# Kernel optimization log

Measured on AMD Instinct MI355X. Metric: run time of the kernel, lower is better.

The kernel has to match this reference:

```python
import jax, jax.numpy as jnp
import numpy as np

B, L, D, H, NS = 8, 1024, 64, 16, 3
DH = D // H          # head dim = 4 (scale = sqrt(4) = 2, matching K_.size(-1)**0.5)
DFF = 4 * D          # 256
EPS = 1e-5


def _bn(x_bld, gamma, beta):
    # BatchNorm1d in training mode on (B, C, L): normalize per-channel over (B, L)
    mean = jnp.mean(x_bld, axis=(0, 1))          # [D]
    var = jnp.mean((x_bld - mean) ** 2, axis=(0, 1))  # biased variance, as torch uses
    return gamma * (x_bld - mean) / jnp.sqrt(var + EPS) + beta


def setup_inputs() -> dict:
    key = jax.random.key(0)
    ks = jax.random.split(key, 12)
    s = 0.05
    inp = {
        "x": jax.random.normal(ks[0], (B, L, D), dtype=jnp.float32),
        # W_embed: Conv1d(64,64,k=1) == linear over channels
        "W_embed": jax.random.normal(ks[1], (D, D), dtype=jnp.float32) * s,
        "b_embed": jnp.zeros((D,), dtype=jnp.float32),
        "g0": jnp.ones((D,), dtype=jnp.float32),
        "be0": jnp.zeros((D,), dtype=jnp.float32),
        # shared attention weights (reused every stack)
        "Wq": jax.random.normal(ks[2], (D, D), dtype=jnp.float32) * s,
        "bq": jnp.zeros((D,), dtype=jnp.float32),
        "Wk": jax.random.normal(ks[3], (D, D), dtype=jnp.float32) * s,
        "bk": jnp.zeros((D,), dtype=jnp.float32),
        "Wv": jax.random.normal(ks[4], (D, D), dtype=jnp.float32) * s,
        "bv": jnp.zeros((D,), dtype=jnp.float32),
        "g_attn": jnp.ones((D,), dtype=jnp.float32),
        "be_attn": jnp.zeros((D,), dtype=jnp.float32),
        # shared feedforward (1x1 convs == channel linears)
        "W1": jax.random.normal(ks[5], (DFF, D), dtype=jnp.float32) * s,
        "b1": jnp.zeros((DFF,), dtype=jnp.float32),
        "W2": jax.random.normal(ks[6], (D, DFF), dtype=jnp.float32) * s,
        "b2": jnp.zeros((D,), dtype=jnp.float32),
        "g_ff": jnp.ones((D,), dtype=jnp.float32),
        "be_ff": jnp.zeros((D,), dtype=jnp.float32),
    }
    return inp


def reference(x, W_embed, b_embed, g0, be0, Wq, bq, Wk, bk, Wv, bv,
              g_attn, be_attn, W1, b1, W2, b2, g_ff, be_ff):
    # input embedding (1x1 conv) + batchnorm
    enc = x @ W_embed.T + b_embed              # [B, L, D]
    enc = _bn(enc, g0, be0)

    for _ in range(NS):  # num_stacks, SAME weights each stack (as in source)
        # --- multi-head attention (ReLU-activated QKV projections) ---
        Q = jax.nn.relu(enc @ Wq.T + bq)        # [B, L, D]
        K = jax.nn.relu(enc @ Wk.T + bk)
        V = jax.nn.relu(enc @ Wv.T + bv)
        q = Q.reshape(B, L, H, DH)
        k = K.reshape(B, L, H, DH)
        v = V.reshape(B, L, H, DH)
        scores = jnp.einsum('blhd,bmhd->bhlm', q, k) / jnp.sqrt(jnp.float32(DH))
        A = jax.nn.softmax(scores, axis=-1)     # [B, H, L, L]
        o = jnp.einsum('bhlm,bmhd->blhd', A, v).reshape(B, L, D)
        o = o + enc                             # residual
        enc = _bn(o, g_attn, be_attn)

        # --- feedforward: conv1d(k=1) -> ReLU -> conv1d(k=1) -> ReLU, residual, BN ---
        h = jax.nn.relu(enc @ W1.T + b1)        # [B, L, 4D]
        h = jax.nn.relu(h @ W2.T + b2)          # [B, L, D]
        h = h + enc                             # residual
        enc = _bn(h, g_ff, be_ff)
    return enc
```

## Files before the change

### kernel.cpp

```cpp
#include <hip/hip_runtime.h>
#include <math.h>

static constexpr int B_ = 8, L_ = 1024, D_ = 64, H_ = 16, DH_ = 4, DFF_ = 256;
static constexpr int M_ = B_ * L_;
static constexpr float EPS_ = 1e-5f;
static constexpr float INV_N_ = 1.0f / (float)M_;
static constexpr int PSTR_ = 128;

typedef _Float16 half4_ __attribute__((ext_vector_type(4)));
typedef __fp16   fp16x2 __attribute__((ext_vector_type(2)));
typedef float    f32x4  __attribute__((ext_vector_type(4)));

__global__ __launch_bounds__(256) void prep_kernel(
    const float* __restrict__ we, const float* __restrict__ wq,
    const float* __restrict__ wk, const float* __restrict__ wv,
    const float* __restrict__ w1, const float* __restrict__ w2,
    _Float16* __restrict__ dst)
{
    int e = blockIdx.x * 256 + threadIdx.x;
    float v;
    if      (e <  4096) v = we[e];
    else if (e <  8192) v = wq[e - 4096];
    else if (e < 12288) v = wk[e - 8192];
    else if (e < 16384) v = wv[e - 12288];
    else if (e < 32768) v = w1[e - 16384];
    else                v = w2[e - 32768];
    dst[e] = (_Float16)v;
}

template<int KT, int AF16, int BN_A, int RELU, int RESID_BN, int STATS, int OUTF16>
__device__ __forceinline__ void linear_mfma(
    const float* __restrict__ Af, const _Float16* __restrict__ Ah,
    const _Float16* __restrict__ Wh,
    const float* __restrict__ bias, const float* __restrict__ resid,
    float* __restrict__ Cf, _Float16* __restrict__ Ch, float outScale,
    int N, int m0, int n0,
    const float* __restrict__ partsIn, int npb,
    const float* __restrict__ gg, const float* __restrict__ bb,
    float* __restrict__ outParts, int blkIdx)
{
    constexpr int CPR = KT / 4;
    __shared__ half4_ Alds[64][CPR + 1];
    __shared__ half4_ Wlds[64][CPR + 1];
    __shared__ float  raw[128];
    __shared__ float  bnsc[64], bnsh[64];
    __shared__ float  wstats[4][128];
    const int t = threadIdx.x;

    if (BN_A || RESID_BN) {
        if (t < 128) {
            const float* pr = partsIn + (size_t)t * PSTR_;
            float a = 0.f;
            for (int j = 0; j < npb; j += 4) {
                float4 v4 = *(const float4*)&pr[j];
                a += v4.x + v4.y + v4.z + v4.w;
            }
            raw[t] = a;
        }
        __syncthreads();
        if (t < 64) {
            float mean = raw[t] * INV_N_;
            float ex2  = raw[64 + t] * INV_N_;
            float rs   = rsqrtf(ex2 - mean * mean + EPS_);
            float s2   = gg[t] * rs;
            bnsc[t] = s2;
            bnsh[t] = bb[t] - mean * s2;
        }
        __syncthreads();
    }

    {
        constexpr int ITERS = (64 * CPR) / 256;
        #pragma unroll
        for (int i = 0; i < ITERS; ++i) {
            int l = i * 256 + t;
            int row = l / CPR, c4 = l % CPR;
            half4_ hv;
            if (AF16) {
                hv = *(const half4_*)&Ah[(size_t)(m0 + row) * KT + c4 * 4];
            } else {
                float4 av = *(const float4*)&Af[(size_t)(m0 + row) * KT + c4 * 4];
                if (BN_A) {
                    int c = c4 * 4;
                    av.x = fmaf(av.x, bnsc[c + 0], bnsh[c + 0]);
                    av.y = fmaf(av.y, bnsc[c + 1], bnsh[c + 1]);
                    av.z = fmaf(av.z, bnsc[c + 2], bnsh[c + 2]);
                    av.w = fmaf(av.w, bnsc[c + 3], bnsh[c + 3]);
                }
                hv = half4_{(_Float16)av.x, (_Float16)av.y,
                            (_Float16)av.z, (_Float16)av.w};
            }
            Alds[row][c4] = hv;
            Wlds[row][c4] = *(const half4_*)&Wh[(size_t)(n0 + row) * KT + c4 * 4];
        }
    }
    __syncthreads();

    const int lane = t & 63, w = t >> 6, g = lane >> 4, ml = lane & 15;

    f32x4 acc[4] = {};
    #pragma unroll
    for (int kci = 0; kci < KT / 16; ++kci) {
        half4_ af = Alds[w * 16 + ml][kci * 4 + g];
        #pragma unroll
        for (int nt = 0; nt < 4; ++nt) {
            half4_ wf = Wlds[nt * 16 + ml][kci * 4 + g];
            acc[nt] = __builtin_amdgcn_mfma_f32_16x16x16f16(wf, af, acc[nt], 0, 0, 0);
        }
    }

    const int m = m0 + w * 16 + ml;
    float sv[4][4], qv[4][4];
    #pragma unroll
    for (int nt = 0; nt < 4; ++nt) {
        const int cb = nt * 16 + 4 * g;
        const int nc = n0 + cb;
        float4 bv4 = *(const float4*)&bias[nc];
        float r0 = acc[nt][0] + bv4.x, r1 = acc[nt][1] + bv4.y;
        float r2 = acc[nt][2] + bv4.z, r3 = acc[nt][3] + bv4.w;
        if (RELU) {
            r0 = fmaxf(r0, 0.f); r1 = fmaxf(r1, 0.f);
            r2 = fmaxf(r2, 0.f); r3 = fmaxf(r3, 0.f);
        }
        if (RESID_BN) {
            float4 rv = *(const float4*)&resid[(size_t)m * N + nc];
            r0 += fmaf(rv.x, bnsc[cb + 0], bnsh[cb + 0]);
            r1 += fmaf(rv.y, bnsc[cb + 1], bnsh[cb + 1]);
            r2 += fmaf(rv.z, bnsc[cb + 2], bnsh[cb + 2]);
            r3 += fmaf(rv.w, bnsc[cb + 3], bnsh[cb + 3]);
        }
        if (OUTF16) {
            half4_ hs = { (_Float16)(r0 * outScale), (_Float16)(r1 * outScale),
                          (_Float16)(r2 * outScale), (_Float16)(r3 * outScale) };
            *(half4_*)&Ch[(size_t)m * N + nc] = hs;
        } else {
            float4 o4 = { r0, r1, r2, r3 };
            *(float4*)&Cf[(size_t)m * N + nc] = o4;
        }
        if (STATS) {
            sv[nt][0] = r0; sv[nt][1] = r1; sv[nt][2] = r2; sv[nt][3] = r3;
            qv[nt][0] = r0 * r0; qv[nt][1] = r1 * r1;
            qv[nt][2] = r2 * r2; qv[nt][3] = r3 * r3;
        }
    }

    if (STATS) {
        #pragma unroll
        for (int d = 1; d <= 8; d <<= 1)
            #pragma unroll
            for (int nt = 0; nt < 4; ++nt)
                #pragma unroll
                for (int r = 0; r < 4; ++r) {
                    sv[nt][r] += __shfl_xor(sv[nt][r], d);
                    qv[nt][r] += __shfl_xor(qv[nt][r], d);
                }
        if (ml == 0) {
            #pragma unroll
            for (int nt = 0; nt < 4; ++nt)
                #pragma unroll
                for (int r = 0; r < 4; ++r) {
                    int ch = nt * 16 + 4 * g + r;
                    wstats[w][ch]      = sv[nt][r];
                    wstats[w][64 + ch] = qv[nt][r];
                }
        }
        __syncthreads();
        if (t < 128) {
            float a = wstats[0][t] + wstats[1][t] + wstats[2][t] + wstats[3][t];
            outParts[(size_t)t * PSTR_ + blkIdx] = a;
        }
    }
}

__global__ __launch_bounds__(256) void embed_kernel(
    const float* __restrict__ x, const _Float16* __restrict__ wemh,
    const float* __restrict__ bias, float* __restrict__ C,
    float* __restrict__ outParts)
{
    linear_mfma<64, 0, 0, 0, 0, 1, 0>(x, nullptr, wemh, bias, nullptr,
                                      C, nullptr, 1.f, 64, blockIdx.x * 64, 0,
                                      nullptr, 0, nullptr, nullptr,
                                      outParts, blockIdx.x);
}

__global__ __launch_bounds__(256) void qkv_kernel(
    const float* __restrict__ tmpA,
    const _Float16* __restrict__ wqh, const float* __restrict__ bq,
    const _Float16* __restrict__ wkh, const float* __restrict__ bk,
    const _Float16* __restrict__ wvh, const float* __restrict__ bv,
    _Float16* __restrict__ qh, _Float16* __restrict__ kh, _Float16* __restrict__ vh,
    const float* __restrict__ partsIn,
    const float* __restrict__ g, const float* __restrict__ be)
{
    const _Float16* W; const float* bias; _Float16* C; float sc2;
    if (blockIdx.y == 0)      { W = wqh; bias = bq; C = qh; sc2 = 0.5f; }
    else if (blockIdx.y == 1) { W = wkh; bias = bk; C = kh; sc2 = 1.f; }
    else                      { W = wvh; bias = bv; C = vh; sc2 = 1.f; }
    linear_mfma<64, 0, 1, 1, 0, 0, 1>(tmpA, nullptr, W, bias, nullptr,
                                      nullptr, C, sc2, 64, blockIdx.x * 64, 0,
                                      partsIn, 128, g, be, nullptr, 0);
}

__global__ __launch_bounds__(256) void ff1_kernel(
    const float* __restrict__ tmpB, const _Float16* __restrict__ w1h,
    const float* __restrict__ b1, _Float16* __restrict__ h1,
    const float* __restrict__ partsB,
    const float* __restrict__ g, const float* __restrict__ be)
{
    linear_mfma<64, 0, 1, 1, 0, 0, 1>(tmpB, nullptr, w1h, b1, nullptr,
                                      nullptr, h1, 1.f, 256,
                                      blockIdx.x * 64, blockIdx.y * 64,
                                      partsB, 64, g, be, nullptr, 0);
}

__global__ __launch_bounds__(256) void ff2_kernel(
    const _Float16* __restrict__ h1, const _Float16* __restrict__ w2h,
    const float* __restrict__ b2, const float* __restrict__ tmpB,
    float* __restrict__ tmpA, const float* __restrict__ partsB,
    const float* __restrict__ g, const float* __restrict__ be,
    float* __restrict__ partsOut)
{
    linear_mfma<256, 1, 0, 1, 1, 1, 0>(nullptr, h1, w2h, b2, tmpB,
                                       tmpA, nullptr, 1.f, 64, blockIdx.x * 64, 0,
                                       partsB, 64, g, be, partsOut, blockIdx.x);
}

__global__ __launch_bounds__(256) void attn_kernel(
    const _Float16* __restrict__ q, const _Float16* __restrict__ k,
    const _Float16* __restrict__ v, const float* __restrict__ encRaw,
    float* __restrict__ out, const float* __restrict__ partsIn,
    const float* __restrict__ gPrev, const float* __restrict__ bPrev,
    float* __restrict__ partsOut)
{
    __shared__ half4_   klds[1024];
    __shared__ _Float16 vstage[4][1040];
    __shared__ half4_   vlds[1024];
    __shared__ float    raw8[8], rsc[4], rsh[4];
    __shared__ float    wred[4][8];

    const int bid = blockIdx.x;
    const int qc  = bid & 7;
    const int h   = (bid >> 3) & 15;
    const int b   = bid >> 7;
    const int t   = threadIdx.x;

    if (t < 8) {
        const int row = (t >> 2) * 64 + 4 * h + (t & 3);
        const float* pr = partsIn + (size_t)row * PSTR_;
        float a = 0.f;
        for (int j = 0; j < 128; j += 4) {
            float4 v4 = *(const float4*)&pr[j];
            a += v4.x + v4.y + v4.z + v4.w;
        }
        raw8[t] = a;
    }

    const size_t baseh = (size_t)b * (L_ * D_) + h * DH_;

    #pragma unroll
    for (int i = 0; i < 4; ++i) {
        int key = i * 256 + t;
        klds[key] = *(const half4_*)&k[baseh + (size_t)key * D_];
        half4_ vv = *(const half4_*)&v[baseh + (size_t)key * D_];
        vstage[0][key] = vv[0]; vstage[1][key] = vv[1];
        vstage[2][key] = vv[2]; vstage[3][key] = vv[3];
    }
    __syncthreads();

    if (t < 4) {
        float mean = raw8[t] * INV_N_;
        float ex2  = raw8[4 + t] * INV_N_;
        float rs   = rsqrtf(ex2 - mean * mean + EPS_);
        float s2   = gPrev[4 * h + t] * rs;
        rsc[t] = s2;
        rsh[t] = bPrev[4 * h + t] - mean * s2;
    }

    #pragma unroll
    for (int i = 0; i < 4; ++i) {
        int e = i * 256 + t;
        int d = e & 3, g2 = (e >> 2) & 3, c = e >> 4;
        int k0 = c * 16 + g2 * 4;
        half4_ hv = { vstage[d][k0 + 0], vstage[d][k0 + 1],
                      vstage[d][k0 + 2], vstage[d][k0 + 3] };
        vlds[e] = hv;
    }
    __syncthreads();

    const int lane = t & 63;
    const int wv2  = t >> 6;
    const int ln16 = lane & 15;
    const int g16  = lane >> 4;
    const int q0   = qc * 128 + wv2 * 32;

    half4_ qf0 = { 0, 0, 0, 0 }, qf1 = { 0, 0, 0, 0 };
    if (lane < 16) {
        qf0 = *(const half4_*)&q[(size_t)(b * L_ + q0 + ln16) * D_ + h * DH_];
        qf1 = *(const half4_*)&q[(size_t)(b * L_ + q0 + 16 + ln16) * D_ + h * DH_];
    }

    const half4_ ones = { (_Float16)1.f, (_Float16)1.f, (_Float16)1.f, (_Float16)1.f };
    const f32x4  fz   = { 0.f, 0.f, 0.f, 0.f };
    f32x4 o0 = fz, o1 = fz;

    #pragma unroll 2
    for (int c = 0; c < 64; ++c) {
        half4_ ka = klds[c * 16 + ln16];
        half4_ va = vlds[c * 16 + g16 * 4 + (ln16 & 3)];
        if (ln16 == 4) va = ones;

        f32x4 s0 = __builtin_amdgcn_mfma_f32_16x16x16f16(ka, qf0, fz, 0, 0, 0);
        f32x4 s1 = __builtin_amdgcn_mfma_f32_16x16x16f16(ka, qf1, fz, 0, 0, 0);

        float e00 = __expf(s0[0]), e01 = __expf(s0[1]);
        float e02 = __expf(s0[2]), e03 = __expf(s0[3]);
        float e10 = __expf(s1[0]), e11 = __expf(s1[1]);
        float e12 = __expf(s1[2]), e13 = __expf(s1[3]);

        fp16x2 a0 = __builtin_amdgcn_cvt_pkrtz(e00, e01);
        fp16x2 b0 = __builtin_amdgcn_cvt_pkrtz(e02, e03);
        fp16x2 a1 = __builtin_amdgcn_cvt_pkrtz(e10, e11);
        fp16x2 b1 = __builtin_amdgcn_cvt_pkrtz(e12, e13);
        half4_ p0 = __builtin_bit_cast(half4_, __builtin_shufflevector(a0, b0, 0, 1, 2, 3));
        half4_ p1 = __builtin_bit_cast(half4_, __builtin_shufflevector(a1, b1, 0, 1, 2, 3));

        o0 = __builtin_amdgcn_mfma_f32_16x16x16f16(va, p0, o0, 0, 0, 0);
        o1 = __builtin_amdgcn_mfma_f32_16x16x16f16(va, p1, o1, 0, 0, 0);
    }

    float ls0 = __shfl(o0[0], 16 + ln16);
    float ls1 = __shfl(o1[0], 16 + ln16);

    float4 r0v = { 0.f, 0.f, 0.f, 0.f }, r1v = r0v;
    if (lane < 16) {
        {
            const size_t gi = (size_t)(b * L_ + q0 + ln16) * D_ + h * DH_;
            const float inv = 1.0f / ls0;
            const float4 e4 = *(const float4*)&encRaw[gi];
            r0v.x = fmaf(o0[0], inv, fmaf(e4.x, rsc[0], rsh[0]));
            r0v.y = fmaf(o0[1], inv, fmaf(e4.y, rsc[1], rsh[1]));
            r0v.z = fmaf(o0[2], inv, fmaf(e4.z, rsc[2], rsh[2]));
            r0v.w = fmaf(o0[3], inv, fmaf(e4.w, rsc[3], rsh[3]));
            *(float4*)&out[gi] = r0v;
        }
        {
            const size_t gi = (size_t)(b * L_ + q0 + 16 + ln16) * D_ + h * DH_;
            const float inv = 1.0f / ls1;
            const float4 e4 = *(const float4*)&encRaw[gi];
            r1v.x = fmaf(o1[0], inv, fmaf(e4.x, rsc[0], rsh[0]));
            r1v.y = fmaf(o1[1], inv, fmaf(e4.y, rsc[1], rsh[1]));
            r1v.z = fmaf(o1[2], inv, fmaf(e4.z, rsc[2], rsh[2]));
            r1v.w = fmaf(o1[3], inv, fmaf(e4.w, rsc[3], rsh[3]));
            *(float4*)&out[gi] = r1v;
        }
    }

    float s4[4] = { r0v.x + r1v.x, r0v.y + r1v.y, r0v.z + r1v.z, r0v.w + r1v.w };
    float q4[4] = { r0v.x*r0v.x + r1v.x*r1v.x, r0v.y*r0v.y + r1v.y*r1v.y,
                    r0v.z*r0v.z + r1v.z*r1v.z, r0v.w*r0v.w + r1v.w*r1v.w };
    #pragma unroll
    for (int d2 = 1; d2 <= 8; d2 <<= 1) {
        #pragma unroll
        for (int j = 0; j < 4; ++j) {
            s4[j] += __shfl_xor(s4[j], d2);
            q4[j] += __shfl_xor(q4[j], d2);
        }
    }
    if (lane == 0) {
        #pragma unroll
        for (int j = 0; j < 4; ++j) { wred[wv2][j] = s4[j]; wred[wv2][4 + j] = q4[j]; }
    }
    __syncthreads();
    if (t < 8) {
        float a = wred[0][t] + wred[1][t] + wred[2][t] + wred[3][t];
        const int row = (t >> 2) * 64 + 4 * h + (t & 3);
        partsOut[(size_t)row * PSTR_ + (b * 8 + qc)] = a;
    }
}

__global__ __launch_bounds__(256) void bn_apply_kernel(
    const float* __restrict__ x, const float* __restrict__ parts,
    const float* __restrict__ gamma, const float* __restrict__ beta,
    float* __restrict__ y)
{
    __shared__ float fstats[128];
    const int t = threadIdx.x;
    if (t < 128) {
        const float* pr = parts + (size_t)t * PSTR_;
        float a = 0.f;
        for (int j = 0; j < 128; j += 4) {
            float4 v4 = *(const float4*)&pr[j];
            a += v4.x + v4.y + v4.z + v4.w;
        }
        fstats[t] = a;
    }
    __syncthreads();

    const int idx = blockIdx.x * 256 + t;
    const int c = (idx & 15) << 2;
    float4 xv = ((const float4*)x)[idx];
    float4 sm = *(const float4*)&fstats[c];
    float4 sq = *(const float4*)&fstats[64 + c];
    float4 g  = *(const float4*)&gamma[c];
    float4 be = *(const float4*)&beta[c];

    float mean[4] = {sm.x * INV_N_, sm.y * INV_N_, sm.z * INV_N_, sm.w * INV_N_};
    float ex2[4]  = {sq.x * INV_N_, sq.y * INV_N_, sq.z * INV_N_, sq.w * INV_N_};
    float xa[4] = {xv.x, xv.y, xv.z, xv.w};
    float ga[4] = {g.x, g.y, g.z, g.w};
    float ba[4] = {be.x, be.y, be.z, be.w};
    float ya[4];
    #pragma unroll
    for (int i = 0; i < 4; ++i) {
        float var = ex2[i] - mean[i] * mean[i];
        float rs = rsqrtf(var + EPS_);
        ya[i] = ga[i] * (xa[i] - mean[i]) * rs + ba[i];
    }
    float4 r = {ya[0], ya[1], ya[2], ya[3]};
    ((float4*)y)[idx] = r;
}

extern "C" void kernel_launch(void* const* d_in, const int* in_sizes, int n_in,
                              void* d_out, int out_size, void* d_ws, size_t ws_size,
                              hipStream_t stream)
{
    const float* x       = (const float*)d_in[0];
    const float* W_embed = (const float*)d_in[1];
    const float* b_embed = (const float*)d_in[2];
    const float* g0      = (const float*)d_in[3];
    const float* be0     = (const float*)d_in[4];
    const float* Wq      = (const float*)d_in[5];
    const float* bq      = (const float*)d_in[6];
    const float* Wk      = (const float*)d_in[7];
    const float* bk      = (const float*)d_in[8];
    const float* Wv      = (const float*)d_in[9];
    const float* bv      = (const float*)d_in[10];
    const float* g_attn  = (const float*)d_in[11];
    const float* be_attn = (const float*)d_in[12];
    const float* W1      = (const float*)d_in[13];
    const float* b1      = (const float*)d_in[14];
    const float* W2      = (const float*)d_in[15];
    const float* b2      = (const float*)d_in[16];
    const float* g_ff    = (const float*)d_in[17];
    const float* be_ff   = (const float*)d_in[18];

    float* ws     = (float*)d_ws;
    float* tmpA   = ws;
    float* tmpB   = ws + 524288;
    float* partsA = ws + 1048576;
    float* partsB = ws + 1064960;
    _Float16* hb  = (_Float16*)(ws + 1081344);
    _Float16* qh  = hb;
    _Float16* kh  = hb + 524288;
    _Float16* vh  = hb + 1048576;
    _Float16* h1  = hb + 1572864;
    _Float16* wemh = hb + 3670016;
    _Float16* wqh  = wemh + 4096;
    _Float16* wkh  = wqh + 4096;
    _Float16* wvh  = wkh + 4096;
    _Float16* w1h  = wvh + 4096;
    _Float16* w2h  = w1h + 16384;
    float* out = (float*)d_out;

    const dim3 blk(256);

    prep_kernel<<<192, blk, 0, stream>>>(W_embed, Wq, Wk, Wv, W1, W2, wemh);
    embed_kernel<<<128, blk, 0, stream>>>(x, wemh, b_embed, tmpA, partsA);

    for (int s = 0; s < 3; ++s) {
        const float* gP  = (s == 0) ? g0  : g_ff;
        const float* beP = (s == 0) ? be0 : be_ff;
        qkv_kernel<<<dim3(128, 3), blk, 0, stream>>>(
            tmpA, wqh, bq, wkh, bk, wvh, bv, qh, kh, vh, partsA, gP, beP);
        attn_kernel<<<1024, blk, 0, stream>>>(
            qh, kh, vh, tmpA, tmpB, partsA, gP, beP, partsB);
        ff1_kernel<<<dim3(128, 4), blk, 0, stream>>>(
            tmpB, w1h, b1, h1, partsB, g_attn, be_attn);
        ff2_kernel<<<128, blk, 0, stream>>>(
            h1, w2h, b2, tmpB, tmpA, partsB, g_attn, be_attn, partsA);
    }
    bn_apply_kernel<<<512, blk, 0, stream>>>(tmpA, partsA, g_ff, be_ff, out);
}
```

Measured before the change: 189.0 us.

## Fuse feedforward linears into one kernel keeping hidden activations in registers

Merges the two feedforward 1x1-conv kernels into a single kernel. The first MFMA output is bias+ReLU'd and packed directly as the A operand of the second MFMA. This removes the global round trip of the 4D-wide hidden tensor and one launch per stack. Weights are read from global/cache rather than staged in LDS. The residual is taken from the fp16 normalized tile in LDS, trading some precision, and only 128 blocks are launched.

```diff
diff --git a/kernel.cpp b/kernel.cpp
--- a/kernel.cpp
+++ b/kernel.cpp
@@ -28,11 +28,10 @@
     dst[e] = (_Float16)v;
 }
 
-template<int KT, int AF16, int BN_A, int RELU, int RESID_BN, int STATS, int OUTF16>
+template<int KT, int BN_A, int RELU, int STATS, int OUTF16>
 __device__ __forceinline__ void linear_mfma(
-    const float* __restrict__ Af, const _Float16* __restrict__ Ah,
-    const _Float16* __restrict__ Wh,
-    const float* __restrict__ bias, const float* __restrict__ resid,
+    const float* __restrict__ Af, const _Float16* __restrict__ Wh,
+    const float* __restrict__ bias,
     float* __restrict__ Cf, _Float16* __restrict__ Ch, float outScale,
     int N, int m0, int n0,
     const float* __restrict__ partsIn, int npb,
@@ -47,7 +46,7 @@
     __shared__ float  wstats[4][128];
     const int t = threadIdx.x;
 
-    if (BN_A || RESID_BN) {
+    if (BN_A) {
         if (t < 128) {
             const float* pr = partsIn + (size_t)t * PSTR_;
             float a = 0.f;
@@ -75,22 +74,16 @@
         for (int i = 0; i < ITERS; ++i) {
             int l = i * 256 + t;
             int row = l / CPR, c4 = l % CPR;
-            half4_ hv;
-            if (AF16) {
-                hv = *(const half4_*)&Ah[(size_t)(m0 + row) * KT + c4 * 4];
-            } else {
-                float4 av = *(const float4*)&Af[(size_t)(m0 + row) * KT + c4 * 4];
-                if (BN_A) {
-                    int c = c4 * 4;
-                    av.x = fmaf(av.x, bnsc[c + 0], bnsh[c + 0]);
-                    av.y = fmaf(av.y, bnsc[c + 1], bnsh[c + 1]);
-                    av.z = fmaf(av.z, bnsc[c + 2], bnsh[c + 2]);
-                    av.w = fmaf(av.w, bnsc[c + 3], bnsh[c + 3]);
-                }
-                hv = half4_{(_Float16)av.x, (_Float16)av.y,
-                            (_Float16)av.z, (_Float16)av.w};
+            float4 av = *(const float4*)&Af[(size_t)(m0 + row) * KT + c4 * 4];
+            if (BN_A) {
+                int c = c4 * 4;
+                av.x = fmaf(av.x, bnsc[c + 0], bnsh[c + 0]);
+                av.y = fmaf(av.y, bnsc[c + 1], bnsh[c + 1]);
+                av.z = fmaf(av.z, bnsc[c + 2], bnsh[c + 2]);
+                av.w = fmaf(av.w, bnsc[c + 3], bnsh[c + 3]);
             }
-            Alds[row][c4] = hv;
+            Alds[row][c4] = half4_{(_Float16)av.x, (_Float16)av.y,
+                                   (_Float16)av.z, (_Float16)av.w};
             Wlds[row][c4] = *(const half4_*)&Wh[(size_t)(n0 + row) * KT + c4 * 4];
         }
     }
@@ -121,13 +114,6 @@
         if (RELU) {
             r0 = fmaxf(r0, 0.f); r1 = fmaxf(r1, 0.f);
             r2 = fmaxf(r2, 0.f); r3 = fmaxf(r3, 0.f);
-        }
-        if (RESID_BN) {
-            float4 rv = *(const float4*)&resid[(size_t)m * N + nc];
-            r0 += fmaf(rv.x, bnsc[cb + 0], bnsh[cb + 0]);
-            r1 += fmaf(rv.y, bnsc[cb + 1], bnsh[cb + 1]);
-            r2 += fmaf(rv.z, bnsc[cb + 2], bnsh[cb + 2]);
-            r3 += fmaf(rv.w, bnsc[cb + 3], bnsh[cb + 3]);
         }
         if (OUTF16) {
             half4_ hs = { (_Float16)(r0 * outScale), (_Float16)(r1 * outScale),
@@ -177,10 +163,10 @@
     const float* __restrict__ bias, float* __restrict__ C,
     float* __restrict__ outParts)
 {
-    linear_mfma<64, 0, 0, 0, 0, 1, 0>(x, nullptr, wemh, bias, nullptr,
-                                      C, nullptr, 1.f, 64, blockIdx.x * 64, 0,
-                                      nullptr, 0, nullptr, nullptr,
-                                      outParts, blockIdx.x);
+    linear_mfma<64, 0, 0, 1, 0>(x, wemh, bias, C, nullptr, 1.f, 64,
+                                blockIdx.x * 64, 0,
+                                nullptr, 0, nullptr, nullptr,
+                                outParts, blockIdx.x);
 }
 
 __global__ __launch_bounds__(256) void qkv_kernel(
@@ -196,33 +182,136 @@
     if (blockIdx.y == 0)      { W = wqh; bias = bq; C = qh; sc2 = 0.5f; }
     else if (blockIdx.y == 1) { W = wkh; bias = bk; C = kh; sc2 = 1.f; }
     else                      { W = wvh; bias = bv; C = vh; sc2 = 1.f; }
-    linear_mfma<64, 0, 1, 1, 0, 0, 1>(tmpA, nullptr, W, bias, nullptr,
-                                      nullptr, C, sc2, 64, blockIdx.x * 64, 0,
-                                      partsIn, 128, g, be, nullptr, 0);
-}
-
-__global__ __launch_bounds__(256) void ff1_kernel(
+    linear_mfma<64, 1, 1, 0, 1>(tmpA, W, bias, nullptr, C, sc2, 64,
+                                blockIdx.x * 64, 0,
+                                partsIn, 128, g, be, nullptr, 0);
+}
+
+__global__ __launch_bounds__(256) void ff_kernel(
     const float* __restrict__ tmpB, const _Float16* __restrict__ w1h,
-    const float* __restrict__ b1, _Float16* __restrict__ h1,
+    const float* __restrict__ b1, const _Float16* __restrict__ w2h,
+    const float* __restrict__ b2, float* __restrict__ tmpA,
     const float* __restrict__ partsB,
-    const float* __restrict__ g, const float* __restrict__ be)
-{
-    linear_mfma<64, 0, 1, 1, 0, 0, 1>(tmpB, nullptr, w1h, b1, nullptr,
-                                      nullptr, h1, 1.f, 256,
-                                      blockIdx.x * 64, blockIdx.y * 64,
-                                      partsB, 64, g, be, nullptr, 0);
-}
-
-__global__ __launch_bounds__(256) void ff2_kernel(
-    const _Float16* __restrict__ h1, const _Float16* __restrict__ w2h,
-    const float* __restrict__ b2, const float* __restrict__ tmpB,
-    float* __restrict__ tmpA, const float* __restrict__ partsB,
-    const float* __restrict__ g, const float* __restrict__ be,
-    float* __restrict__ partsOut)
-{
-    linear_mfma<256, 1, 0, 1, 1, 1, 0>(nullptr, h1, w2h, b2, tmpB,
-                                       tmpA, nullptr, 1.f, 64, blockIdx.x * 64, 0,
-                                       partsB, 64, g, be, partsOut, blockIdx.x);
+    const float* __restrict__ gg, const float* __restrict__ bb,
+    float* __restrict__ outParts)
+{
+    __shared__ half4_ Alds[64][17];
+    __shared__ float  raw[128];
+    __shared__ float  bnsc[64], bnsh[64];
+    __shared__ float  wstats[4][128];
+    const int t  = threadIdx.x;
+    const int m0 = blockIdx.x * 64;
+
+    if (t < 128) {
+        const float* pr = partsB + (size_t)t * PSTR_;
+        float a = 0.f;
+        for (int j = 0; j < 64; j += 4) {
+            float4 v4 = *(const float4*)&pr[j];
+            a += v4.x + v4.y + v4.z + v4.w;
+        }
+        raw[t] = a;
+    }
+    __syncthreads();
+    if (t < 64) {
+        float mean = raw[t] * INV_N_;
+        float ex2  = raw[64 + t] * INV_N_;
+        float rs   = rsqrtf(ex2 - mean * mean + EPS_);
+        float s2   = gg[t] * rs;
+        bnsc[t] = s2;
+        bnsh[t] = bb[t] - mean * s2;
+    }
+    __syncthreads();
+
+    #pragma unroll
+    for (int i = 0; i < 4; ++i) {
+        int l = i * 256 + t;
+        int row = l >> 4, c4 = l & 15;
+        float4 av = *(const float4*)&tmpB[(size_t)(m0 + row) * 64 + c4 * 4];
+        int c = c4 * 4;
+        av.x = fmaf(av.x, bnsc[c + 0], bnsh[c + 0]);
+        av.y = fmaf(av.y, bnsc[c + 1], bnsh[c + 1]);
+        av.z = fmaf(av.z, bnsc[c + 2], bnsh[c + 2]);
+        av.w = fmaf(av.w, bnsc[c + 3], bnsh[c + 3]);
+        Alds[row][c4] = half4_{(_Float16)av.x, (_Float16)av.y,
+                               (_Float16)av.z, (_Float16)av.w};
+    }
+    __syncthreads();
+
+    const int lane = t & 63, w = t >> 6, g = lane >> 4, ml = lane & 15;
+
+    f32x4 acc1[16] = {};
+    #pragma unroll
+    for (int kci = 0; kci < 4; ++kci) {
+        half4_ af = Alds[w * 16 + ml][kci * 4 + g];
+        #pragma unroll
+        for (int nt = 0; nt < 16; ++nt) {
+            half4_ wf = *(const half4_*)&w1h[(size_t)(nt * 16 + ml) * 64 + kci * 16 + 4 * g];
+            acc1[nt] = __builtin_amdgcn_mfma_f32_16x16x16f16(wf, af, acc1[nt], 0, 0, 0);
+        }
+    }
+
+    f32x4 acc2[4] = {};
+    #pragma unroll
+    for (int kci2 = 0; kci2 < 16; ++kci2) {
+        float4 b1v = *(const float4*)&b1[kci2 * 16 + 4 * g];
+        float e0 = fmaxf(acc1[kci2][0] + b1v.x, 0.f);
+        float e1 = fmaxf(acc1[kci2][1] + b1v.y, 0.f);
+        float e2 = fmaxf(acc1[kci2][2] + b1v.z, 0.f);
+        float e3 = fmaxf(acc1[kci2][3] + b1v.w, 0.f);
+        fp16x2 lo = __builtin_amdgcn_cvt_pkrtz(e0, e1);
+        fp16x2 hi = __builtin_amdgcn_cvt_pkrtz(e2, e3);
+        half4_ af2 = __builtin_bit_cast(half4_, __builtin_shufflevector(lo, hi, 0, 1, 2, 3));
+        #pragma unroll
+        for (int nt2 = 0; nt2 < 4; ++nt2) {
+            half4_ wf2 = *(const half4_*)&w2h[(size_t)(nt2 * 16 + ml) * 256 + kci2 * 16 + 4 * g];
+            acc2[nt2] = __builtin_amdgcn_mfma_f32_16x16x16f16(wf2, af2, acc2[nt2], 0, 0, 0);
+        }
+    }
+
+    const int m = m0 + w * 16 + ml;
+    float sv[4][4], qv[4][4];
+    #pragma unroll
+    for (int nt2 = 0; nt2 < 4; ++nt2) {
+        const int cb = nt2 * 16 + 4 * g;
+        float4 b2v = *(const float4*)&b2[cb];
+        float r0 = acc2[nt2][0] + b2v.x, r1 = acc2[nt2][1] + b2v.y;
+        float r2 = acc2[nt2][2] + b2v.z, r3 = acc2[nt2][3] + b2v.w;
+        r0 = fmaxf(r0, 0.f); r1 = fmaxf(r1, 0.f);
+        r2 = fmaxf(r2, 0.f); r3 = fmaxf(r3, 0.f);
+        half4_ rr = Alds[w * 16 + ml][nt2 * 4 + g];
+        r0 += (float)rr[0]; r1 += (float)rr[1];
+        r2 += (float)rr[2]; r3 += (float)rr[3];
+        float4 o4 = { r0, r1, r2, r3 };
+        *(float4*)&tmpA[(size_t)m * 64 + cb] = o4;
+        sv[nt2][0] = r0; sv[nt2][1] = r1; sv[nt2][2] = r2; sv[nt2][3] = r3;
+        qv[nt2][0] = r0 * r0; qv[nt2][1] = r1 * r1;
+        qv[nt2][2] = r2 * r2; qv[nt2][3] = r3 * r3;
+    }
+
+    #pragma unroll
+    for (int d = 1; d <= 8; d <<= 1)
+        #pragma unroll
+        for (int nt2 = 0; nt2 < 4; ++nt2)
+            #pragma unroll
+            for (int r = 0; r < 4; ++r) {
+                sv[nt2][r] += __shfl_xor(sv[nt2][r], d);
+                qv[nt2][r] += __shfl_xor(qv[nt2][r], d);
+            }
+    if (ml == 0) {
+        #pragma unroll
+        for (int nt2 = 0; nt2 < 4; ++nt2)
+            #pragma unroll
+            for (int r = 0; r < 4; ++r) {
+                int ch = nt2 * 16 + 4 * g + r;
+                wstats[w][ch]      = sv[nt2][r];
+                wstats[w][64 + ch] = qv[nt2][r];
+            }
+    }
+    __syncthreads();
+    if (t < 128) {
+        float a = wstats[0][t] + wstats[1][t] + wstats[2][t] + wstats[3][t];
+        outParts[(size_t)t * PSTR_ + blockIdx.x] = a;
+    }
 }
 
 __global__ __launch_bounds__(256) void attn_kernel(
@@ -453,8 +542,7 @@
     _Float16* qh  = hb;
     _Float16* kh  = hb + 524288;
     _Float16* vh  = hb + 1048576;
-    _Float16* h1  = hb + 1572864;
-    _Float16* wemh = hb + 3670016;
+    _Float16* wemh = hb + 1572864;
     _Float16* wqh  = wemh + 4096;
     _Float16* wkh  = wqh + 4096;
     _Float16* wvh  = wkh + 4096;
@@ -474,10 +562,8 @@
             tmpA, wqh, bq, wkh, bk, wvh, bv, qh, kh, vh, partsA, gP, beP);
         attn_kernel<<<1024, blk, 0, stream>>>(
             qh, kh, vh, tmpA, tmpB, partsA, gP, beP, partsB);
-        ff1_kernel<<<dim3(128, 4), blk, 0, stream>>>(
-            tmpB, w1h, b1, h1, partsB, g_attn, be_attn);
-        ff2_kernel<<<128, blk, 0, stream>>>(
-            h1, w2h, b2, tmpB, tmpA, partsB, g_attn, be_attn, partsA);
+        ff_kernel<<<128, blk, 0, stream>>>(
+            tmpB, w1h, b1, w2h, b2, tmpA, partsB, g_attn, be_attn, partsA);
     }
     bn_apply_kernel<<<512, blk, 0, stream>>>(tmpA, partsA, g_ff, be_ff, out);
 }
```

New measurement: 210.5 us. 1.11x slower.
